# Performance work log

Hardware: AMD Instinct MI355X
Metric: run time of the kernel (lower is better)

Reference implementation:

```python
import jax, jax.numpy as jnp
import numpy as np
from jax import lax

GAMMA = 1.0
B = 10            # forced by qnn_arch[0]=10 via w1 @ x in feedforward
N_TRAIN = 8192    # kernel support set size


def setup_inputs() -> dict:
    key = jax.random.key(0)
    ks = jax.random.split(key, 20)
    x = jax.random.normal(ks[0], (B, 3, 250, 250), jnp.float32)
    # CNN params (He-ish scale)
    conv1_w = jax.random.normal(ks[1], (6, 3, 5, 5), jnp.float32) * 0.1
    conv1_b = jax.random.normal(ks[2], (6,), jnp.float32) * 0.01
    conv2_w = jax.random.normal(ks[3], (15, 6, 3, 3), jnp.float32) * 0.1
    conv2_b = jax.random.normal(ks[4], (15,), jnp.float32) * 0.01
    fc1_w = jax.random.normal(ks[5], (120, 55815), jnp.float32) * 0.004
    fc1_b = jax.random.normal(ks[6], (120,), jnp.float32) * 0.01
    fc2_w = jax.random.normal(ks[7], (84, 120), jnp.float32) * 0.09
    fc2_b = jax.random.normal(ks[8], (84,), jnp.float32) * 0.01
    fc3_w = jax.random.normal(ks[9], (1, 84), jnp.float32) * 0.1
    fc3_b = jax.random.normal(ks[10], (1,), jnp.float32) * 0.01
    # QNN weights (original uses plain randn)
    qnn_w1 = jax.random.normal(ks[11], (20, 10), jnp.float32)
    qnn_w2 = jax.random.normal(ks[12], (5, 20), jnp.float32)
    # Precomputed training states: tanh(w2 @ tanh(w1 @ f)) per random feature f
    feats = jax.random.normal(ks[13], (N_TRAIN, 10), jnp.float32)
    train_states = jnp.tanh(jnp.tanh(feats @ qnn_w1.T) @ qnn_w2.T)  # [N_TRAIN, 5]
    kcls_w = jax.random.normal(ks[14], (2, N_TRAIN), jnp.float32) * 0.01
    kcls_b = jax.random.normal(ks[15], (2,), jnp.float32) * 0.01
    return {
        'x': x,
        'conv1_w': conv1_w, 'conv1_b': conv1_b,
        'conv2_w': conv2_w, 'conv2_b': conv2_b,
        'fc1_w': fc1_w, 'fc1_b': fc1_b,
        'fc2_w': fc2_w, 'fc2_b': fc2_b,
        'fc3_w': fc3_w, 'fc3_b': fc3_b,
        'qnn_w1': qnn_w1, 'qnn_w2': qnn_w2,
        'train_states': train_states,
        'kcls_w': kcls_w, 'kcls_b': kcls_b,
    }


def _conv(h, w, b, stride, pad):
    out = lax.conv_general_dilated(
        h, w, (stride, stride), [(pad, pad), (pad, pad)],
        dimension_numbers=('NCHW', 'OIHW', 'NCHW'))
    return out + b[None, :, None, None]


def _maxpool_2s1(h):
    return lax.reduce_window(h, -jnp.inf, lax.max, (1, 1, 2, 2), (1, 1, 1, 1), 'VALID')


def reference(x, conv1_w, conv1_b, conv2_w, conv2_b, fc1_w, fc1_b,
              fc2_w, fc2_b, fc3_w, fc3_b, qnn_w1, qnn_w2,
              train_states, kcls_w, kcls_b):
    h = jax.nn.relu(_conv(x, conv1_w, conv1_b, 2, 1))   # [10,6,124,124]
    h = _maxpool_2s1(h)                                 # [10,6,123,123]
    h = jax.nn.relu(_conv(h, conv2_w, conv2_b, 2, 1))   # [10,15,62,62]
    h = _maxpool_2s1(h)                                 # [10,15,61,61]
    h = h.reshape(h.shape[0], -1)                       # [10,55815]
    h = jax.nn.relu(h @ fc1_w.T + fc1_b)                # [10,120]
    h = jax.nn.relu(h @ fc2_w.T + fc2_b)                # [10,84]
    h = h @ fc3_w.T + fc3_b                             # [10,1]
    # QNN feedforward: batch dim B=10 is consumed as the qnn input dim
    s = jnp.tanh(qnn_w1 @ h)                            # [20,1]
    s = jnp.tanh(qnn_w2 @ s)                            # [5,1]
    fs = s[:, 0]                                        # [5]
    # Batched RBF kernel against all train states (replaces the Python .item() loop)
    d2 = jnp.sum((fs[None, :] - train_states) ** 2, axis=-1)  # [N_TRAIN]
    K = jnp.exp(-GAMMA * d2)                            # [N_TRAIN]
    out = K[None, :] @ kcls_w.T + kcls_b                # [1,2]
    return out
```

## Files before the change

### kernel.cpp

```cpp
#include <hip/hip_runtime.h>


__global__ __launch_bounds__(256) void convpool1_k(
    const float* __restrict__ x, const float* __restrict__ w,
    const float* __restrict__ bias, float* __restrict__ out ) {
    const int b   = blockIdx.x;
    const int py0 = blockIdx.y * 2;
    const int px0 = blockIdx.z * 62;
    const int n_py = (123 - py0) < 2 ? (123 - py0) : 2;
    const int n_oy = n_py + 1;
    const int iy0 = 2 * py0 - 1;
    const int ix0 = 2 * px0 - 1;

    __shared__ float sx[3][9][132];
    __shared__ float so[6][3][64];

    const int tid = threadIdx.x;

    for (int j = tid; j < 3 * 9 * 129; j += 256) {
        int col = j % 129;
        int r   = (j / 129) % 9;
        int ic  = j / (129 * 9);
        int ix = ix0 + col, iy = iy0 + r;
        float v = 0.f;
        if ((unsigned)ix < 250u && (unsigned)iy < 250u)
            v = x[((size_t)(b * 3 + ic) * 250 + iy) * 250 + ix];
        sx[ic][r][col] = v;
    }
    __syncthreads();

    for (int p = tid; p < n_oy * 63; p += 256) {
        int oxl = p % 63;
        int oyl = p / 63;
        if (px0 + oxl < 124) {
            float acc[6];
            #pragma unroll
            for (int o = 0; o < 6; ++o) acc[o] = bias[o];
            #pragma unroll
            for (int ic = 0; ic < 3; ++ic) {
                #pragma unroll
                for (int ky = 0; ky < 5; ++ky) {
                    const float* xr = &sx[ic][2 * oyl + ky][2 * oxl];
                    #pragma unroll
                    for (int kx = 0; kx < 5; ++kx) {
                        float xv = xr[kx];
                        #pragma unroll
                        for (int o = 0; o < 6; ++o)
                            acc[o] += w[((o * 3 + ic) * 5 + ky) * 5 + kx] * xv;
                    }
                }
            }
            #pragma unroll
            for (int o = 0; o < 6; ++o) so[o][oyl][oxl] = fmaxf(acc[o], 0.f);
        }
    }
    __syncthreads();

    for (int j = tid; j < 6 * 2 * 62; j += 256) {
        int pxl = j % 62;
        int pyl = (j / 62) & 1;
        int oc  = j / 124;
        int px = px0 + pxl, py = py0 + pyl;
        if (pyl < n_py && px < 123) {
            float v = fmaxf(fmaxf(so[oc][pyl][pxl],     so[oc][pyl][pxl + 1]),
                            fmaxf(so[oc][pyl + 1][pxl], so[oc][pyl + 1][pxl + 1]));
            out[((size_t)(b * 6 + oc) * 123 + py) * 123 + px] = v;
        }
    }
}

__global__ __launch_bounds__(128) void convpool2_k(
    const float* __restrict__ in , const float* __restrict__ w,
    const float* __restrict__ bias, float* __restrict__ out ) {
    const int b   = blockIdx.x;
    const int py0 = blockIdx.y * 2;
    const int px0 = blockIdx.z * 31;
    const int n_py = (61 - py0) < 2 ? (61 - py0) : 2;
    const int n_oy = n_py + 1;
    const int iy0 = 2 * py0 - 1;
    const int ix0 = 2 * px0 - 1;

    __shared__ float sx[6][7][68];
    __shared__ float so[15][3][32];

    const int tid = threadIdx.x;

    for (int j = tid; j < 6 * 7 * 65; j += 128) {
        int col = j % 65;
        int r   = (j / 65) % 7;
        int ic  = j / (65 * 7);
        int ix = ix0 + col, iy = iy0 + r;
        float v = 0.f;
        if ((unsigned)ix < 123u && (unsigned)iy < 123u)
            v = in[((size_t)(b * 6 + ic) * 123 + iy) * 123 + ix];
        sx[ic][r][col] = v;
    }
    __syncthreads();

    for (int p = tid; p < n_oy * 32; p += 128) {
        int oxl = p % 32;
        int oyl = p / 32;
        if (px0 + oxl < 62) {
            float acc[15];
            #pragma unroll
            for (int o = 0; o < 15; ++o) acc[o] = bias[o];
            #pragma unroll
            for (int ic = 0; ic < 6; ++ic) {
                #pragma unroll
                for (int ky = 0; ky < 3; ++ky) {
                    const float* xr = &sx[ic][2 * oyl + ky][2 * oxl];
                    #pragma unroll
                    for (int kx = 0; kx < 3; ++kx) {
                        float xv = xr[kx];
                        #pragma unroll
                        for (int o = 0; o < 15; ++o)
                            acc[o] += w[((o * 6 + ic) * 3 + ky) * 3 + kx] * xv;
                    }
                }
            }
            #pragma unroll
            for (int o = 0; o < 15; ++o) so[o][oyl][oxl] = fmaxf(acc[o], 0.f);
        }
    }
    __syncthreads();

    for (int j = tid; j < 15 * 2 * 31; j += 128) {
        int pxl = j % 31;
        int pyl = (j / 31) & 1;
        int oc  = j / 62;
        int px = px0 + pxl, py = py0 + pyl;
        if (pyl < n_py && px < 61) {
            float v = fmaxf(fmaxf(so[oc][pyl][pxl],     so[oc][pyl][pxl + 1]),
                            fmaxf(so[oc][pyl + 1][pxl], so[oc][pyl + 1][pxl + 1]));
            out[((size_t)(b * 15 + oc) * 61 + py) * 61 + px] = v;
        }
    }
}

#define FC1_K      55815
#define FC1_CHUNK  768
#define FC1_NC     73
#define FC1_RT     15

__global__ __launch_bounds__(256) void fc1_partial_k(
    const float* __restrict__ act ,
    const float* __restrict__ w   ,
    float* __restrict__ partials  ) {
    int rt  = blockIdx.x;
    int c   = blockIdx.y;
    int tid = threadIdx.x;
    int wave = tid >> 6, lane = tid & 63;
    int k0 = c * FC1_CHUNK;
    int k1 = k0 + FC1_CHUNK; if (k1 > FC1_K) k1 = FC1_K;
    int r0 = rt * 8 + wave * 2;
    const float* w0 = w + (size_t)r0 * FC1_K;
    const float* w1 = w + (size_t)(r0 + 1) * FC1_K;

    float acc0[10], acc1[10];
    #pragma unroll
    for (int b = 0; b < 10; ++b) { acc0[b] = 0.f; acc1[b] = 0.f; }

    for (int k = k0 + lane; k < k1; k += 64) {
        float a[10];
        #pragma unroll
        for (int b = 0; b < 10; ++b) a[b] = act[(size_t)b * FC1_K + k];
        float wv0 = w0[k];
        float wv1 = w1[k];
        #pragma unroll
        for (int b = 0; b < 10; ++b) {
            acc0[b] += wv0 * a[b];
            acc1[b] += wv1 * a[b];
        }
    }
    #pragma unroll
    for (int b = 0; b < 10; ++b) {
        float v0 = acc0[b], v1 = acc1[b];
        for (int off = 32; off > 0; off >>= 1) {
            v0 += __shfl_down(v0, off);
            v1 += __shfl_down(v1, off);
        }
        if (lane == 0) {
            size_t base = ((size_t)c * 120 + r0) * 10;
            partials[base + b]      = v0;
            partials[base + 10 + b] = v1;
        }
    }
}

__global__ __launch_bounds__(128) void fc1_reduce_k(
    const float* __restrict__ part ,
    const float* __restrict__ bias,
    float* __restrict__ out1 ) {
    int idx = blockIdx.x * 128 + threadIdx.x;
    if (idx >= 1200) return;
    int row = idx / 10, b = idx % 10;
    float s = 0.f;
    #pragma unroll 8
    for (int c = 0; c < FC1_NC; ++c) s += part[((size_t)c * 120 + row) * 10 + b];
    out1[b * 120 + row] = fmaxf(s + bias[row], 0.f);
}

__global__ __launch_bounds__(256) void head2_k(
    const float* __restrict__ out1 ,
    const float* __restrict__ fc2_w, const float* __restrict__ fc2_b,
    const float* __restrict__ fc3_w, const float* __restrict__ fc3_b,
    const float* __restrict__ qw1, const float* __restrict__ qw2,
    float* __restrict__ fs_out ) {
    __shared__ float s_act[1200];
    __shared__ float s_w[84][121];
    __shared__ float s_fc2[840];
    __shared__ float s_h3[10], s_s1[20];
    int tid = threadIdx.x;

    for (int i = tid; i < 1200; i += 256) s_act[i] = out1[i];
    for (int i = tid; i < 84 * 120; i += 256) {
        int j = i / 120, k = i % 120;
        s_w[j][k] = fc2_w[i];
    }
    __syncthreads();

    for (int p = tid; p < 840; p += 256) {
        int b = p / 84, j = p % 84;
        float acc = fc2_b[j];
        #pragma unroll 4
        for (int k = 0; k < 120; ++k) acc += s_act[b * 120 + k] * s_w[j][k];
        s_fc2[b * 84 + j] = fmaxf(acc, 0.f);
    }
    __syncthreads();

    if (tid < 10) {
        float acc = fc3_b[0];
        for (int j = 0; j < 84; ++j) acc += s_fc2[tid * 84 + j] * fc3_w[j];
        s_h3[tid] = acc;
    }
    __syncthreads();
    if (tid < 20) {
        float acc = 0.f;
        for (int b = 0; b < 10; ++b) acc += qw1[tid * 10 + b] * s_h3[b];
        s_s1[tid] = tanhf(acc);
    }
    __syncthreads();
    if (tid < 5) {
        float acc = 0.f;
        for (int j = 0; j < 20; ++j) acc += qw2[tid * 20 + j] * s_s1[j];
        fs_out[tid] = tanhf(acc);
    }
}

__global__ __launch_bounds__(128) void cls_partial_k(
    const float* __restrict__ fs,
    const float* __restrict__ ts ,
    const float* __restrict__ kw ,
    float* __restrict__ partials ) {
    int tid = threadIdx.x;
    int n = blockIdx.x * 128 + tid;
    __shared__ float s_fs[5];
    if (tid < 5) s_fs[tid] = fs[tid];
    __syncthreads();
    float f0 = s_fs[0], f1 = s_fs[1], f2 = s_fs[2], f3 = s_fs[3], f4 = s_fs[4];
    const float* t = ts + (size_t)n * 5;
    float d0 = f0 - t[0], d1 = f1 - t[1], d2 = f2 - t[2], d3 = f3 - t[3], d4 = f4 - t[4];
    float Kv = expf(-(d0 * d0 + d1 * d1 + d2 * d2 + d3 * d3 + d4 * d4));
    float a0 = Kv * kw[n];
    float a1 = Kv * kw[8192 + n];
    for (int off = 32; off > 0; off >>= 1) {
        a0 += __shfl_down(a0, off);
        a1 += __shfl_down(a1, off);
    }
    __shared__ float l0[2], l1[2];
    int wave = tid >> 6, lane = tid & 63;
    if (lane == 0) { l0[wave] = a0; l1[wave] = a1; }
    __syncthreads();
    if (tid == 0) {
        partials[blockIdx.x * 2 + 0] = l0[0] + l0[1];
        partials[blockIdx.x * 2 + 1] = l1[0] + l1[1];
    }
}

__global__ void cls_final_k(const float* __restrict__ partials,
                            const float* __restrict__ kb, float* __restrict__ out) {
    int c = threadIdx.x;
    if (c < 2) {
        float acc = kb[c];
        for (int i = 0; i < 64; ++i) acc += partials[i * 2 + c];
        out[c] = acc;
    }
}

extern "C" void kernel_launch(void* const* d_in, const int* in_sizes, int n_in,
                              void* d_out, int out_size, void* d_ws, size_t ws_size,
                              hipStream_t stream) {
    const float* x        = (const float*)d_in[0];
    const float* conv1_w  = (const float*)d_in[1];
    const float* conv1_b  = (const float*)d_in[2];
    const float* conv2_w  = (const float*)d_in[3];
    const float* conv2_b  = (const float*)d_in[4];
    const float* fc1_w    = (const float*)d_in[5];
    const float* fc1_b    = (const float*)d_in[6];
    const float* fc2_w    = (const float*)d_in[7];
    const float* fc2_b    = (const float*)d_in[8];
    const float* fc3_w    = (const float*)d_in[9];
    const float* fc3_b    = (const float*)d_in[10];
    const float* qnn_w1   = (const float*)d_in[11];
    const float* qnn_w2   = (const float*)d_in[12];
    const float* tstates  = (const float*)d_in[13];
    const float* kcls_w   = (const float*)d_in[14];
    const float* kcls_b   = (const float*)d_in[15];

    float* ws = (float*)d_ws;
    float* p1       = ws;
    float* p2       = p1 + 907740;
    float* fc1_part = p2 + 558150;
    float* out1     = fc1_part + 87600;
    float* fs       = out1 + 1200;
    float* partials = fs + 8;

    convpool1_k<<<dim3(10, 62, 2), 256, 0, stream>>>(x, conv1_w, conv1_b, p1);
    convpool2_k<<<dim3(10, 31, 2), 128, 0, stream>>>(p1, conv2_w, conv2_b, p2);
    fc1_partial_k<<<dim3(FC1_RT, FC1_NC), 256, 0, stream>>>(p2, fc1_w, fc1_part);
    fc1_reduce_k<<<10, 128, 0, stream>>>(fc1_part, fc1_b, out1);
    head2_k<<<1, 256, 0, stream>>>(out1, fc2_w, fc2_b, fc3_w, fc3_b, qnn_w1, qnn_w2, fs);
    cls_partial_k<<<64, 128, 0, stream>>>(fs, tstates, kcls_w, partials);
    cls_final_k<<<1, 64, 0, stream>>>(partials, kcls_b, (float*)d_out);
}
```

Measured before the change: 85.68 us.

## Split conv1 input by parity, vectorize fc1 loads, fuse head kernels

Conv1 stores input columns in separate even and odd shared arrays, which removes stride-2 bank conflicts, and uses smaller 4-row by 31-column tiles with 128 threads. The second pooled activation is written with a padded per-batch stride so fc1 can read it with aligned float4 loads across k. The fc1 reduce, fc2 and fc3 steps are fused into one kernel with one block per batch, and the QNN layers are fused into the RBF classifier kernel, cutting two launches and the single-block fc2 bottleneck. The cost is that every classifier block recomputes the tiny QNN, and fc1 now relies on the padded stride and on 16-byte alignment.

```diff
diff --git a/kernel.cpp b/kernel.cpp
--- a/kernel.cpp
+++ b/kernel.cpp
@@ -1,67 +1,68 @@
 #include <hip/hip_runtime.h>
 
 
-__global__ __launch_bounds__(256) void convpool1_k(
+#define ACT_STRIDE 55816
+
+__global__ __launch_bounds__(128) void convpool1_k(
     const float* __restrict__ x, const float* __restrict__ w,
     const float* __restrict__ bias, float* __restrict__ out ) {
     const int b   = blockIdx.x;
-    const int py0 = blockIdx.y * 2;
-    const int px0 = blockIdx.z * 62;
-    const int n_py = (123 - py0) < 2 ? (123 - py0) : 2;
-    const int n_oy = n_py + 1;
+    const int py0 = blockIdx.y * 4;
+    const int px0 = blockIdx.z * 31;
     const int iy0 = 2 * py0 - 1;
     const int ix0 = 2 * px0 - 1;
 
-    __shared__ float sx[3][9][132];
-    __shared__ float so[6][3][64];
+    __shared__ float sxe[3][13][34];
+    __shared__ float sxo[3][13][34];
+    __shared__ float so[6][5][32];
 
     const int tid = threadIdx.x;
 
-    for (int j = tid; j < 3 * 9 * 129; j += 256) {
-        int col = j % 129;
-        int r   = (j / 129) % 9;
-        int ic  = j / (129 * 9);
-        int ix = ix0 + col, iy = iy0 + r;
+    for (int j = tid; j < 3 * 13 * 67; j += 128) {
+        int c  = j % 67;
+        int r  = (j / 67) % 13;
+        int ic = j / (67 * 13);
+        int ix = ix0 + c, iy = iy0 + r;
         float v = 0.f;
         if ((unsigned)ix < 250u && (unsigned)iy < 250u)
             v = x[((size_t)(b * 3 + ic) * 250 + iy) * 250 + ix];
-        sx[ic][r][col] = v;
-    }
-    __syncthreads();
-
-    for (int p = tid; p < n_oy * 63; p += 256) {
-        int oxl = p % 63;
-        int oyl = p / 63;
-        if (px0 + oxl < 124) {
-            float acc[6];
-            #pragma unroll
-            for (int o = 0; o < 6; ++o) acc[o] = bias[o];
-            #pragma unroll
-            for (int ic = 0; ic < 3; ++ic) {
+        if (c & 1) sxo[ic][r][c >> 1] = v;
+        else       sxe[ic][r][c >> 1] = v;
+    }
+    __syncthreads();
+
+    for (int p = tid; p < 5 * 32; p += 128) {
+        int oxl = p & 31;
+        int oyl = p >> 5;
+        float acc[6];
+        #pragma unroll
+        for (int o = 0; o < 6; ++o) acc[o] = bias[o];
+        #pragma unroll
+        for (int ic = 0; ic < 3; ++ic) {
+            #pragma unroll
+            for (int ky = 0; ky < 5; ++ky) {
+                int r = 2 * oyl + ky;
                 #pragma unroll
-                for (int ky = 0; ky < 5; ++ky) {
-                    const float* xr = &sx[ic][2 * oyl + ky][2 * oxl];
+                for (int kx = 0; kx < 5; ++kx) {
+                    float xv = (kx & 1) ? sxo[ic][r][oxl + (kx >> 1)]
+                                        : sxe[ic][r][oxl + (kx >> 1)];
                     #pragma unroll
-                    for (int kx = 0; kx < 5; ++kx) {
-                        float xv = xr[kx];
-                        #pragma unroll
-                        for (int o = 0; o < 6; ++o)
-                            acc[o] += w[((o * 3 + ic) * 5 + ky) * 5 + kx] * xv;
-                    }
+                    for (int o = 0; o < 6; ++o)
+                        acc[o] += w[((o * 3 + ic) * 5 + ky) * 5 + kx] * xv;
                 }
             }
-            #pragma unroll
-            for (int o = 0; o < 6; ++o) so[o][oyl][oxl] = fmaxf(acc[o], 0.f);
-        }
-    }
-    __syncthreads();
-
-    for (int j = tid; j < 6 * 2 * 62; j += 256) {
-        int pxl = j % 62;
-        int pyl = (j / 62) & 1;
+        }
+        #pragma unroll
+        for (int o = 0; o < 6; ++o) so[o][oyl][oxl] = fmaxf(acc[o], 0.f);
+    }
+    __syncthreads();
+
+    for (int j = tid; j < 6 * 4 * 31; j += 128) {
+        int pxl = j % 31;
+        int pyl = (j / 31) & 3;
         int oc  = j / 124;
         int px = px0 + pxl, py = py0 + pyl;
-        if (pyl < n_py && px < 123) {
+        if (px < 123 && py < 123) {
             float v = fmaxf(fmaxf(so[oc][pyl][pxl],     so[oc][pyl][pxl + 1]),
                             fmaxf(so[oc][pyl + 1][pxl], so[oc][pyl + 1][pxl + 1]));
             out[((size_t)(b * 6 + oc) * 123 + py) * 123 + px] = v;
@@ -98,8 +99,8 @@
     __syncthreads();
 
     for (int p = tid; p < n_oy * 32; p += 128) {
-        int oxl = p % 32;
-        int oyl = p / 32;
+        int oxl = p & 31;
+        int oyl = p >> 5;
         if (px0 + oxl < 62) {
             float acc[15];
             #pragma unroll
@@ -132,7 +133,7 @@
         if (pyl < n_py && px < 61) {
             float v = fmaxf(fmaxf(so[oc][pyl][pxl],     so[oc][pyl][pxl + 1]),
                             fmaxf(so[oc][pyl + 1][pxl], so[oc][pyl + 1][pxl + 1]));
-            out[((size_t)(b * 15 + oc) * 61 + py) * 61 + px] = v;
+            out[(size_t)b * ACT_STRIDE + ((size_t)oc * 61 + py) * 61 + px] = v;
         }
     }
 }
@@ -160,16 +161,29 @@
     #pragma unroll
     for (int b = 0; b < 10; ++b) { acc0[b] = 0.f; acc1[b] = 0.f; }
 
-    for (int k = k0 + lane; k < k1; k += 64) {
-        float a[10];
-        #pragma unroll
-        for (int b = 0; b < 10; ++b) a[b] = act[(size_t)b * FC1_K + k];
-        float wv0 = w0[k];
-        float wv1 = w1[k];
-        #pragma unroll
-        for (int b = 0; b < 10; ++b) {
-            acc0[b] += wv0 * a[b];
-            acc1[b] += wv1 * a[b];
+    for (int k = k0 + lane * 4; k < k1; k += 256) {
+        if (k + 4 <= k1) {
+            float4 a4[10];
+            #pragma unroll
+            for (int b = 0; b < 10; ++b)
+                a4[b] = *reinterpret_cast<const float4*>(act + (size_t)b * ACT_STRIDE + k);
+            float w00 = w0[k], w01 = w0[k + 1], w02 = w0[k + 2], w03 = w0[k + 3];
+            float w10 = w1[k], w11 = w1[k + 1], w12 = w1[k + 2], w13 = w1[k + 3];
+            #pragma unroll
+            for (int b = 0; b < 10; ++b) {
+                acc0[b] += w00 * a4[b].x + w01 * a4[b].y + w02 * a4[b].z + w03 * a4[b].w;
+                acc1[b] += w10 * a4[b].x + w11 * a4[b].y + w12 * a4[b].z + w13 * a4[b].w;
+            }
+        } else {
+            for (int j = 0; j < k1 - k; ++j) {
+                float wv0 = w0[k + j], wv1 = w1[k + j];
+                #pragma unroll
+                for (int b = 0; b < 10; ++b) {
+                    float av = act[(size_t)b * ACT_STRIDE + k + j];
+                    acc0[b] += wv0 * av;
+                    acc1[b] += wv1 * av;
+                }
+            }
         }
     }
     #pragma unroll
@@ -187,52 +201,45 @@
     }
 }
 
-__global__ __launch_bounds__(128) void fc1_reduce_k(
-    const float* __restrict__ part ,
-    const float* __restrict__ bias,
-    float* __restrict__ out1 ) {
-    int idx = blockIdx.x * 128 + threadIdx.x;
-    if (idx >= 1200) return;
-    int row = idx / 10, b = idx % 10;
-    float s = 0.f;
-    #pragma unroll 8
-    for (int c = 0; c < FC1_NC; ++c) s += part[((size_t)c * 120 + row) * 10 + b];
-    out1[b * 120 + row] = fmaxf(s + bias[row], 0.f);
-}
-
-__global__ __launch_bounds__(256) void head2_k(
-    const float* __restrict__ out1 ,
+__global__ __launch_bounds__(128) void fcA_k(
+    const float* __restrict__ part , const float* __restrict__ fc1_b,
     const float* __restrict__ fc2_w, const float* __restrict__ fc2_b,
     const float* __restrict__ fc3_w, const float* __restrict__ fc3_b,
+    float* __restrict__ h3 ) {
+    const int b = blockIdx.x;
+    const int tid = threadIdx.x;
+    __shared__ float s_act[120];
+    __shared__ float s_fc2[84];
+
+    if (tid < 120) {
+        float s = 0.f;
+        for (int c = 0; c < FC1_NC; ++c) s += part[((size_t)c * 120 + tid) * 10 + b];
+        s_act[tid] = fmaxf(s + fc1_b[tid], 0.f);
+    }
+    __syncthreads();
+    if (tid < 84) {
+        float acc = fc2_b[tid];
+        #pragma unroll 4
+        for (int k = 0; k < 120; ++k) acc += s_act[k] * fc2_w[tid * 120 + k];
+        s_fc2[tid] = fmaxf(acc, 0.f);
+    }
+    __syncthreads();
+    if (tid < 64) {
+        float v = s_fc2[tid] * fc3_w[tid];
+        if (tid < 20) v += s_fc2[tid + 64] * fc3_w[tid + 64];
+        for (int off = 32; off > 0; off >>= 1) v += __shfl_down(v, off);
+        if (tid == 0) h3[b] = v + fc3_b[0];
+    }
+}
+
+__global__ __launch_bounds__(128) void clsB_k(
+    const float* __restrict__ h3 ,
     const float* __restrict__ qw1, const float* __restrict__ qw2,
-    float* __restrict__ fs_out ) {
-    __shared__ float s_act[1200];
-    __shared__ float s_w[84][121];
-    __shared__ float s_fc2[840];
-    __shared__ float s_h3[10], s_s1[20];
+    const float* __restrict__ ts , const float* __restrict__ kw ,
+    float* __restrict__ partials ) {
     int tid = threadIdx.x;
-
-    for (int i = tid; i < 1200; i += 256) s_act[i] = out1[i];
-    for (int i = tid; i < 84 * 120; i += 256) {
-        int j = i / 120, k = i % 120;
-        s_w[j][k] = fc2_w[i];
-    }
-    __syncthreads();
-
-    for (int p = tid; p < 840; p += 256) {
-        int b = p / 84, j = p % 84;
-        float acc = fc2_b[j];
-        #pragma unroll 4
-        for (int k = 0; k < 120; ++k) acc += s_act[b * 120 + k] * s_w[j][k];
-        s_fc2[b * 84 + j] = fmaxf(acc, 0.f);
-    }
-    __syncthreads();
-
-    if (tid < 10) {
-        float acc = fc3_b[0];
-        for (int j = 0; j < 84; ++j) acc += s_fc2[tid * 84 + j] * fc3_w[j];
-        s_h3[tid] = acc;
-    }
+    __shared__ float s_h3[10], s_s1[20], s_fs[5];
+    if (tid < 10) s_h3[tid] = h3[tid];
     __syncthreads();
     if (tid < 20) {
         float acc = 0.f;
@@ -243,21 +250,12 @@
     if (tid < 5) {
         float acc = 0.f;
         for (int j = 0; j < 20; ++j) acc += qw2[tid * 20 + j] * s_s1[j];
-        fs_out[tid] = tanhf(acc);
-    }
-}
-
-__global__ __launch_bounds__(128) void cls_partial_k(
-    const float* __restrict__ fs,
-    const float* __restrict__ ts ,
-    const float* __restrict__ kw ,
-    float* __restrict__ partials ) {
-    int tid = threadIdx.x;
+        s_fs[tid] = tanhf(acc);
+    }
+    __syncthreads();
+
+    float f0 = s_fs[0], f1 = s_fs[1], f2 = s_fs[2], f3 = s_fs[3], f4 = s_fs[4];
     int n = blockIdx.x * 128 + tid;
-    __shared__ float s_fs[5];
-    if (tid < 5) s_fs[tid] = fs[tid];
-    __syncthreads();
-    float f0 = s_fs[0], f1 = s_fs[1], f2 = s_fs[2], f3 = s_fs[3], f4 = s_fs[4];
     const float* t = ts + (size_t)n * 5;
     float d0 = f0 - t[0], d1 = f1 - t[1], d2 = f2 - t[2], d3 = f3 - t[3], d4 = f4 - t[4];
     float Kv = expf(-(d0 * d0 + d1 * d1 + d2 * d2 + d3 * d3 + d4 * d4));
@@ -277,8 +275,8 @@
     }
 }
 
-__global__ void cls_final_k(const float* __restrict__ partials,
-                            const float* __restrict__ kb, float* __restrict__ out) {
+__global__ void clsC_k(const float* __restrict__ partials,
+                       const float* __restrict__ kb, float* __restrict__ out) {
     int c = threadIdx.x;
     if (c < 2) {
         float acc = kb[c];
@@ -310,16 +308,14 @@
     float* ws = (float*)d_ws;
     float* p1       = ws;
     float* p2       = p1 + 907740;
-    float* fc1_part = p2 + 558150;
-    float* out1     = fc1_part + 87600;
-    float* fs       = out1 + 1200;
-    float* partials = fs + 8;
-
-    convpool1_k<<<dim3(10, 62, 2), 256, 0, stream>>>(x, conv1_w, conv1_b, p1);
+    float* fc1_part = p2 + 558160;
+    float* h3       = fc1_part + 87600;
+    float* partials = h3 + 16;
+
+    convpool1_k<<<dim3(10, 31, 4), 128, 0, stream>>>(x, conv1_w, conv1_b, p1);
     convpool2_k<<<dim3(10, 31, 2), 128, 0, stream>>>(p1, conv2_w, conv2_b, p2);
     fc1_partial_k<<<dim3(FC1_RT, FC1_NC), 256, 0, stream>>>(p2, fc1_w, fc1_part);
-    fc1_reduce_k<<<10, 128, 0, stream>>>(fc1_part, fc1_b, out1);
-    head2_k<<<1, 256, 0, stream>>>(out1, fc2_w, fc2_b, fc3_w, fc3_b, qnn_w1, qnn_w2, fs);
-    cls_partial_k<<<64, 128, 0, stream>>>(fs, tstates, kcls_w, partials);
-    cls_final_k<<<1, 64, 0, stream>>>(partials, kcls_b, (float*)d_out);
-}
+    fcA_k<<<10, 128, 0, stream>>>(fc1_part, fc1_b, fc2_w, fc2_b, fc3_w, fc3_b, h3);
+    clsB_k<<<64, 128, 0, stream>>>(h3, qnn_w1, qnn_w2, tstates, kcls_w, partials);
+    clsC_k<<<1, 64, 0, stream>>>(partials, kcls_b, (float*)d_out);
+}
```

Result: slower. 90.31 us (+5.4%).
